# Kernel tuning notes

Measured on AMD Instinct MI355X. Metric: run time of the kernel, lower is better.

The kernel has to match this reference:

```python
import jax, jax.numpy as jnp
import numpy as np

B = 128            # fixed by min(128, len(sample)) loop
NODES_PER_GRAPH = 100
N_NODES = B * NODES_PER_GRAPH
HID = 512          # args.num_hidden
EMB = 1024         # pretrained embedding dim (t_linear in_features)
TWEET_VOCAB = 300000
DESC_VOCAB = 150000
EPS = 1e-5


def setup_inputs() -> dict:
    key = jax.random.key(0)
    ks = jax.random.split(key, 12)
    sample = jnp.stack([
        jax.random.randint(ks[0], (B,), 0, DESC_VOCAB),
        jax.random.randint(ks[1], (B,), 0, TWEET_VOCAB),
        jax.random.randint(ks[2], (B,), 0, DESC_VOCAB),
    ], axis=1)  # [B,3] int
    # sorted node->graph assignment; every graph has >=2 nodes so u_idx+1 is valid
    graph_batch = jnp.repeat(jnp.arange(B), NODES_PER_GRAPH)  # [N_NODES]
    p_feature = jax.random.normal(ks[3], (N_NODES, HID), dtype=jnp.float32)
    tweet_emb = jax.random.normal(ks[4], (TWEET_VOCAB, EMB), dtype=jnp.float32) * 0.02
    desc_emb = jax.random.normal(ks[5], (DESC_VOCAB, EMB), dtype=jnp.float32) * 0.02
    t_w = jax.random.normal(ks[6], (HID, EMB), dtype=jnp.float32) / np.sqrt(EMB)
    t_b = jnp.zeros((HID,), dtype=jnp.float32)
    w1 = jax.random.normal(ks[7], (256, 3 * HID), dtype=jnp.float32) / np.sqrt(3 * HID)
    b1 = jnp.zeros((256,), dtype=jnp.float32)
    gamma = jnp.ones((256,), dtype=jnp.float32)
    beta = jnp.zeros((256,), dtype=jnp.float32)
    w2 = jax.random.normal(ks[8], (1, 256), dtype=jnp.float32) / np.sqrt(256)
    b2 = jnp.zeros((1,), dtype=jnp.float32)
    return {"sample": sample, "graph_batch": graph_batch, "p_feature": p_feature,
            "tweet_emb": tweet_emb, "desc_emb": desc_emb, "t_w": t_w, "t_b": t_b,
            "w1": w1, "b1": b1, "gamma": gamma, "beta": beta, "w2": w2, "b2": b2}


def reference(sample, graph_batch, p_feature, tweet_emb, desc_emb,
              t_w, t_b, w1, b1, gamma, beta, w2, b2):
    # torch.nonzero(batch == i)[0] -> first node index of graph i;
    # graph_batch is sorted, so this is a searchsorted (replaces the 128-iter loop)
    u_idx = jnp.searchsorted(graph_batch, jnp.arange(B))  # [B]
    v_idx = u_idx + 1
    u_feat = p_feature[u_idx]  # [B, HID]
    v_feat = p_feature[v_idx]  # [B, HID]

    t = lambda e: e @ t_w.T + t_b  # Linear(1024 -> HID)
    inp = jnp.concatenate([
        u_feat + t(desc_emb[sample[:, 0]]),
        t(tweet_emb[sample[:, 1]]),
        v_feat + t(desc_emb[sample[:, 2]]),
    ], axis=1)  # [B, 3*HID]

    h = inp @ w1.T + b1  # [B, 256]
    # BatchNorm1d in training mode: biased batch statistics
    mu = jnp.mean(h, axis=0)
    var = jnp.mean((h - mu) ** 2, axis=0)
    h = (h - mu) * jax.lax.rsqrt(var + EPS) * gamma + beta
    # Dropout treated as identity (eval / deterministic reference)
    h = jax.nn.relu(h)
    return jax.nn.sigmoid(h @ w2.T + b2)  # [B, 1]
```

## Files before the change

kernel.cpp:

```cpp
#include <hip/hip_runtime.h>
#include <math.h>

#define BB 128
#define HID 512
#define EMB 1024
#define N1 1536
#define N2 256

typedef __attribute__((ext_vector_type(8))) __bf16 bf16x8;
typedef __attribute__((ext_vector_type(4))) __bf16 bf16x4;
typedef __attribute__((ext_vector_type(4))) float fx4;

#define OFF_ABUF 0
#define OFF_TWB  786432
#define OFF_W1B  1835008
#define OFF_INPB 2621440
#define OFF_P1   3014656
#define OFF_P2   6160384
#define OFF_H    6684672
#define OFF_SC   6815744
#define OFF_SH   6816768
#define OFF_UIDX 6817792

__device__ __forceinline__ fx4 mfma16(bf16x8 a, bf16x8 b, fx4 c) {
    return __builtin_amdgcn_mfma_f32_16x16x32_bf16(a, b, c, 0, 0, 0);
}

__device__ __forceinline__ int lds_idx(int row, int g) {
    return row * 64 + ((g ^ (row & 7)) * 8);
}

__global__ __launch_bounds__(256)
void kA_prep(const int* __restrict__ sample, const int* __restrict__ gb, int n_nodes,
             const float* __restrict__ tweet_emb, const float* __restrict__ desc_emb,
             const float* __restrict__ t_w, const float* __restrict__ w1,
             __bf16* __restrict__ Abuf, __bf16* __restrict__ twb,
             __bf16* __restrict__ w1b, int* __restrict__ uidx)
{
    const int blk = blockIdx.x;
    const int t   = threadIdx.x;

    if (blk < 384) {
        const int s = blk >> 7, b = blk & 127;
        const int id = sample[b * 3 + s];
        const float* src = (s == 1) ? (tweet_emb + (size_t)id * EMB)
                                    : (desc_emb + (size_t)id * EMB);
        float4 v = *(const float4*)(src + t * 4);
        bf16x4 o = {(__bf16)v.x, (__bf16)v.y, (__bf16)v.z, (__bf16)v.w};
        *(bf16x4*)(Abuf + (size_t)blk * EMB + t * 4) = o;
    } else if (blk < 896) {
        const int r = blk - 384;
        float4 v = *(const float4*)(t_w + (size_t)r * EMB + t * 4);
        bf16x4 o = {(__bf16)v.x, (__bf16)v.y, (__bf16)v.z, (__bf16)v.w};
        *(bf16x4*)(twb + (size_t)r * EMB + t * 4) = o;
    } else if (blk < 1152) {
        const int r = blk - 896;
        for (int i = t; i < 384; i += 256) {
            float4 v = *(const float4*)(w1 + (size_t)r * N1 + i * 4);
            bf16x4 o = {(__bf16)v.x, (__bf16)v.y, (__bf16)v.z, (__bf16)v.w};
            *(bf16x4*)(w1b + (size_t)r * N1 + i * 4) = o;
        }
    } else {
        const int n = (blk - 1152) * 256 + t;
        if (n < n_nodes) {
            const int g = gb[n];
            if (n == 0 || gb[n - 1] != g) uidx[g] = n;
        }
    }
}

__global__ __launch_bounds__(256)
void kB_gemm1(const __bf16* __restrict__ Abuf, const __bf16* __restrict__ twb,
              float* __restrict__ part1)
{
    const int n0 = blockIdx.x * 64;
    const int m0 = blockIdx.y * 64;
    const int ks = blockIdx.z;
    const int t  = threadIdx.x;
    const int wid = t >> 6, l = t & 63;
    const int mbase = (wid >> 1) * 32, nbase = (wid & 1) * 32;

    __shared__ __bf16 Alds[64 * 64];
    __shared__ __bf16 Blds[64 * 64];

    const int srow = t >> 2;
    const int g0   = (t & 3) * 2;

    fx4 acc[2][2] = {};

    bf16x8 av0, av1, bv0, bv1;
    {
        const int k0 = ks * 256;
        const __bf16* ap = Abuf + (size_t)(m0 + srow) * EMB + k0 + g0 * 8;
        const __bf16* bp = twb  + (size_t)(n0 + srow) * EMB + k0 + g0 * 8;
        av0 = *(const bf16x8*)ap; av1 = *(const bf16x8*)(ap + 8);
        bv0 = *(const bf16x8*)bp; bv1 = *(const bf16x8*)(bp + 8);
    }

    for (int kt = 0; kt < 4; ++kt) {
        __syncthreads();
        *(bf16x8*)&Alds[lds_idx(srow, g0)]     = av0;
        *(bf16x8*)&Alds[lds_idx(srow, g0 + 1)] = av1;
        *(bf16x8*)&Blds[lds_idx(srow, g0)]     = bv0;
        *(bf16x8*)&Blds[lds_idx(srow, g0 + 1)] = bv1;
        __syncthreads();

        if (kt < 3) {
            const int k0 = ks * 256 + (kt + 1) * 64;
            const __bf16* ap = Abuf + (size_t)(m0 + srow) * EMB + k0 + g0 * 8;
            const __bf16* bp = twb  + (size_t)(n0 + srow) * EMB + k0 + g0 * 8;
            av0 = *(const bf16x8*)ap; av1 = *(const bf16x8*)(ap + 8);
            bv0 = *(const bf16x8*)bp; bv1 = *(const bf16x8*)(bp + 8);
        }

        #pragma unroll
        for (int kq = 0; kq < 2; ++kq) {
            const int g = kq * 4 + (l >> 4);
            bf16x8 a0 = *(const bf16x8*)&Alds[lds_idx(mbase +      (l & 15), g)];
            bf16x8 a1 = *(const bf16x8*)&Alds[lds_idx(mbase + 16 + (l & 15), g)];
            bf16x8 b0 = *(const bf16x8*)&Blds[lds_idx(nbase +      (l & 15), g)];
            bf16x8 b1 = *(const bf16x8*)&Blds[lds_idx(nbase + 16 + (l & 15), g)];
            acc[0][0] = mfma16(a0, b0, acc[0][0]);
            acc[0][1] = mfma16(a0, b1, acc[0][1]);
            acc[1][0] = mfma16(a1, b0, acc[1][0]);
            acc[1][1] = mfma16(a1, b1, acc[1][1]);
        }
    }

    float* dst = part1 + (size_t)ks * (384 * 512);
    #pragma unroll
    for (int mi = 0; mi < 2; ++mi)
        #pragma unroll
        for (int ni = 0; ni < 2; ++ni) {
            const int row = m0 + mbase + mi * 16 + (l >> 4) * 4;
            const int col = n0 + nbase + ni * 16 + (l & 15);
            #pragma unroll
            for (int j = 0; j < 4; ++j)
                dst[(size_t)(row + j) * 512 + col] = acc[mi][ni][j];
        }
}

__global__ __launch_bounds__(256)
void kC_comb1(const float* __restrict__ part1, const float* __restrict__ t_b,
              const float* __restrict__ p_feature, const int* __restrict__ uidx,
              __bf16* __restrict__ inp_bf)
{
    const int t = threadIdx.x;
    const int m = blockIdx.x * 2 + (t >> 7);
    const int j0 = (t & 127) * 4;
    const int s = m >> 7, b = m & 127;

    float4 v = *(const float4*)(part1 + (size_t)m * 512 + j0);
    #pragma unroll
    for (int p = 1; p < 4; ++p) {
        float4 q = *(const float4*)(part1 + (size_t)p * (384 * 512) + (size_t)m * 512 + j0);
        v.x += q.x; v.y += q.y; v.z += q.z; v.w += q.w;
    }
    float4 tb = *(const float4*)(t_b + j0);
    v.x += tb.x; v.y += tb.y; v.z += tb.z; v.w += tb.w;
    if (s != 1) {
        const int node = (s == 0) ? uidx[b] : (uidx[b] + 1);
        float4 pf = *(const float4*)(p_feature + (size_t)node * HID + j0);
        v.x += pf.x; v.y += pf.y; v.z += pf.z; v.w += pf.w;
    }
    bf16x4 o = {(__bf16)v.x, (__bf16)v.y, (__bf16)v.z, (__bf16)v.w};
    *(bf16x4*)(inp_bf + (size_t)m * 512 + j0) = o;
}

__global__ __launch_bounds__(256)
void kD_gemm2(const __bf16* __restrict__ inp_bf, const __bf16* __restrict__ w1b,
              float* __restrict__ part2)
{
    const int n0 = blockIdx.x * 64;
    const int m0 = blockIdx.y * 64;
    const int ks = blockIdx.z;
    const int t  = threadIdx.x;
    const int wid = t >> 6, l = t & 63;
    const int mbase = (wid >> 1) * 32, nbase = (wid & 1) * 32;

    __shared__ __bf16 Alds[64 * 64];
    __shared__ __bf16 Blds[64 * 64];

    const int srow = t >> 2;
    const int g0   = (t & 3) * 2;

    fx4 acc[2][2] = {};

    bf16x8 av0, av1, bv0, bv1;
    {
        const int k0 = ks * 384;
        const __bf16* ap = inp_bf + (size_t)((k0 >> 9) * 128 + m0 + srow) * HID + (k0 & 511) + g0 * 8;
        const __bf16* bp = w1b + (size_t)(n0 + srow) * N1 + k0 + g0 * 8;
        av0 = *(const bf16x8*)ap; av1 = *(const bf16x8*)(ap + 8);
        bv0 = *(const bf16x8*)bp; bv1 = *(const bf16x8*)(bp + 8);
    }

    for (int kt = 0; kt < 6; ++kt) {
        __syncthreads();
        *(bf16x8*)&Alds[lds_idx(srow, g0)]     = av0;
        *(bf16x8*)&Alds[lds_idx(srow, g0 + 1)] = av1;
        *(bf16x8*)&Blds[lds_idx(srow, g0)]     = bv0;
        *(bf16x8*)&Blds[lds_idx(srow, g0 + 1)] = bv1;
        __syncthreads();

        if (kt < 5) {
            const int k0 = ks * 384 + (kt + 1) * 64;
            const __bf16* ap = inp_bf + (size_t)((k0 >> 9) * 128 + m0 + srow) * HID + (k0 & 511) + g0 * 8;
            const __bf16* bp = w1b + (size_t)(n0 + srow) * N1 + k0 + g0 * 8;
            av0 = *(const bf16x8*)ap; av1 = *(const bf16x8*)(ap + 8);
            bv0 = *(const bf16x8*)bp; bv1 = *(const bf16x8*)(bp + 8);
        }

        #pragma unroll
        for (int kq = 0; kq < 2; ++kq) {
            const int g = kq * 4 + (l >> 4);
            bf16x8 a0 = *(const bf16x8*)&Alds[lds_idx(mbase +      (l & 15), g)];
            bf16x8 a1 = *(const bf16x8*)&Alds[lds_idx(mbase + 16 + (l & 15), g)];
            bf16x8 b0 = *(const bf16x8*)&Blds[lds_idx(nbase +      (l & 15), g)];
            bf16x8 b1 = *(const bf16x8*)&Blds[lds_idx(nbase + 16 + (l & 15), g)];
            acc[0][0] = mfma16(a0, b0, acc[0][0]);
            acc[0][1] = mfma16(a0, b1, acc[0][1]);
            acc[1][0] = mfma16(a1, b0, acc[1][0]);
            acc[1][1] = mfma16(a1, b1, acc[1][1]);
        }
    }

    float* dst = part2 + (size_t)ks * (128 * 256);
    #pragma unroll
    for (int mi = 0; mi < 2; ++mi)
        #pragma unroll
        for (int ni = 0; ni < 2; ++ni) {
            const int row = m0 + mbase + mi * 16 + (l >> 4) * 4;
            const int col = n0 + nbase + ni * 16 + (l & 15);
            #pragma unroll
            for (int j = 0; j < 4; ++j)
                dst[(size_t)(row + j) * 256 + col] = acc[mi][ni][j];
        }
}

__global__ __launch_bounds__(256)
void kE_stats(const float* __restrict__ part2, const float* __restrict__ b1,
              const float* __restrict__ gamma, const float* __restrict__ beta,
              float* __restrict__ hbuf, float* __restrict__ scale,
              float* __restrict__ shift)
{
    const int bl = blockIdx.x;
    const int t  = threadIdx.x;
    const int j  = bl * 32 + (t & 31);
    const int q  = t >> 5;

    const float bias = b1[j];
    float sum = 0.f, sq = 0.f;
    for (int i = 0; i < 16; ++i) {
        const int b = q * 16 + i;
        float v = bias;
        #pragma unroll
        for (int p = 0; p < 4; ++p)
            v += part2[(size_t)p * (128 * 256) + b * N2 + j];
        hbuf[b * N2 + j] = v;
        sum += v;
        sq  += v * v;
    }

    __shared__ float s_sum[8][32];
    __shared__ float s_sq[8][32];
    s_sum[q][t & 31] = sum;
    s_sq[q][t & 31]  = sq;
    __syncthreads();

    if (t < 32) {
        float S = 0.f, Q = 0.f;
        #pragma unroll
        for (int q2 = 0; q2 < 8; ++q2) { S += s_sum[q2][t]; Q += s_sq[q2][t]; }
        const float mu  = S * (1.0f / 128.0f);
        const float var = Q * (1.0f / 128.0f) - mu * mu;
        const float rs  = rsqrtf(var + 1e-5f);
        const int jj = bl * 32 + t;
        const float sc = gamma[jj] * rs;
        scale[jj] = sc;
        shift[jj] = beta[jj] - mu * sc;
    }
}

__global__ __launch_bounds__(256)
void kF_out(const float* __restrict__ hbuf, const float* __restrict__ scale,
            const float* __restrict__ shift, const float* __restrict__ w2,
            const float* __restrict__ b2, float* __restrict__ out)
{
    const int t  = threadIdx.x;
    const int wv = t >> 6;
    const int l  = t & 63;
    const int b0 = blockIdx.x * 8 + wv * 2;

    #pragma unroll
    for (int rr = 0; rr < 2; ++rr) {
        const int b = b0 + rr;
        float acc = 0.f;
        #pragma unroll
        for (int i = 0; i < 4; ++i) {
            const int j = l + i * 64;
            float x = hbuf[b * N2 + j] * scale[j] + shift[j];
            x = fmaxf(x, 0.f);
            acc += x * w2[j];
        }
        #pragma unroll
        for (int off = 32; off; off >>= 1) acc += __shfl_xor(acc, off);
        if (l == 0) out[b] = 1.0f / (1.0f + expf(-(acc + b2[0])));
    }
}

extern "C" void kernel_launch(void* const* d_in, const int* in_sizes, int n_in,
                              void* d_out, int out_size, void* d_ws, size_t ws_size,
                              hipStream_t stream) {
    const int*   sample    = (const int*)  d_in[0];
    const int*   gb        = (const int*)  d_in[1];
    const float* p_feature = (const float*)d_in[2];
    const float* tweet_emb = (const float*)d_in[3];
    const float* desc_emb  = (const float*)d_in[4];
    const float* t_w       = (const float*)d_in[5];
    const float* t_b       = (const float*)d_in[6];
    const float* w1        = (const float*)d_in[7];
    const float* b1        = (const float*)d_in[8];
    const float* gamma     = (const float*)d_in[9];
    const float* beta      = (const float*)d_in[10];
    const float* w2        = (const float*)d_in[11];
    const float* b2        = (const float*)d_in[12];
    float* out = (float*)d_out;

    char* ws = (char*)d_ws;
    __bf16* Abuf   = (__bf16*)(ws + OFF_ABUF);
    __bf16* twb    = (__bf16*)(ws + OFF_TWB);
    __bf16* w1b    = (__bf16*)(ws + OFF_W1B);
    __bf16* inp_bf = (__bf16*)(ws + OFF_INPB);
    float*  part1  = (float*)(ws + OFF_P1);
    float*  part2  = (float*)(ws + OFF_P2);
    float*  hbuf   = (float*)(ws + OFF_H);
    float*  scale  = (float*)(ws + OFF_SC);
    float*  shift  = (float*)(ws + OFF_SH);
    int*    uidx   = (int*)  (ws + OFF_UIDX);

    const int n_nodes = in_sizes[1];
    const int scatter_blocks = (n_nodes + 255) / 256;

    kA_prep<<<1152 + scatter_blocks, 256, 0, stream>>>(sample, gb, n_nodes,
        tweet_emb, desc_emb, t_w, w1, Abuf, twb, w1b, uidx);
    kB_gemm1<<<dim3(8, 6, 4), 256, 0, stream>>>(Abuf, twb, part1);
    kC_comb1<<<192, 256, 0, stream>>>(part1, t_b, p_feature, uidx, inp_bf);
    kD_gemm2<<<dim3(4, 2, 4), 256, 0, stream>>>(inp_bf, w1b, part2);
    kE_stats<<<8, 256, 0, stream>>>(part2, b1, gamma, beta, hbuf, scale, shift);
    kF_out<<<16, 256, 0, stream>>>(hbuf, scale, shift, w2, b2, out);
}
```

Measured before the change: 27.79 us.

## Fuse bf16 conversion, gather and bias epilogue into GEMM kernels

Measured after the change: 43.60 us. 56.9% more time.

```diff
diff --git a/kernel.cpp b/kernel.cpp
--- a/kernel.cpp
+++ b/kernel.cpp
@@ -1,26 +1,18 @@
 #include <hip/hip_runtime.h>
 #include <math.h>
 
-#define BB 128
 #define HID 512
 #define EMB 1024
 #define N1 1536
 #define N2 256
 
 typedef __attribute__((ext_vector_type(8))) __bf16 bf16x8;
-typedef __attribute__((ext_vector_type(4))) __bf16 bf16x4;
 typedef __attribute__((ext_vector_type(4))) float fx4;
 
-#define OFF_ABUF 0
-#define OFF_TWB  786432
-#define OFF_W1B  1835008
-#define OFF_INPB 2621440
-#define OFF_P1   3014656
-#define OFF_P2   6160384
-#define OFF_H    6684672
-#define OFF_SC   6815744
-#define OFF_SH   6816768
-#define OFF_UIDX 6817792
+#define OFF_INPB 0
+#define OFF_P2   393216
+#define OFF_SC   917504
+#define OFF_SH   918528
 
 __device__ __forceinline__ fx4 mfma16(bf16x8 a, bf16x8 b, fx4 c) {
     return __builtin_amdgcn_mfma_f32_16x16x32_bf16(a, b, c, 0, 0, 0);
@@ -30,74 +22,66 @@
     return row * 64 + ((g ^ (row & 7)) * 8);
 }
 
+__device__ __forceinline__ bf16x8 cvt8(float4 a, float4 b) {
+    bf16x8 r;
+    r[0] = (__bf16)a.x; r[1] = (__bf16)a.y; r[2] = (__bf16)a.z; r[3] = (__bf16)a.w;
+    r[4] = (__bf16)b.x; r[5] = (__bf16)b.y; r[6] = (__bf16)b.z; r[7] = (__bf16)b.w;
+    return r;
+}
+
 __global__ __launch_bounds__(256)
-void kA_prep(const int* __restrict__ sample, const int* __restrict__ gb, int n_nodes,
-             const float* __restrict__ tweet_emb, const float* __restrict__ desc_emb,
-             const float* __restrict__ t_w, const float* __restrict__ w1,
-             __bf16* __restrict__ Abuf, __bf16* __restrict__ twb,
-             __bf16* __restrict__ w1b, int* __restrict__ uidx)
-{
-    const int blk = blockIdx.x;
-    const int t   = threadIdx.x;
-
-    if (blk < 384) {
-        const int s = blk >> 7, b = blk & 127;
-        const int id = sample[b * 3 + s];
-        const float* src = (s == 1) ? (tweet_emb + (size_t)id * EMB)
-                                    : (desc_emb + (size_t)id * EMB);
-        float4 v = *(const float4*)(src + t * 4);
-        bf16x4 o = {(__bf16)v.x, (__bf16)v.y, (__bf16)v.z, (__bf16)v.w};
-        *(bf16x4*)(Abuf + (size_t)blk * EMB + t * 4) = o;
-    } else if (blk < 896) {
-        const int r = blk - 384;
-        float4 v = *(const float4*)(t_w + (size_t)r * EMB + t * 4);
-        bf16x4 o = {(__bf16)v.x, (__bf16)v.y, (__bf16)v.z, (__bf16)v.w};
-        *(bf16x4*)(twb + (size_t)r * EMB + t * 4) = o;
-    } else if (blk < 1152) {
-        const int r = blk - 896;
-        for (int i = t; i < 384; i += 256) {
-            float4 v = *(const float4*)(w1 + (size_t)r * N1 + i * 4);
-            bf16x4 o = {(__bf16)v.x, (__bf16)v.y, (__bf16)v.z, (__bf16)v.w};
-            *(bf16x4*)(w1b + (size_t)r * N1 + i * 4) = o;
-        }
-    } else {
-        const int n = (blk - 1152) * 256 + t;
-        if (n < n_nodes) {
-            const int g = gb[n];
-            if (n == 0 || gb[n - 1] != g) uidx[g] = n;
-        }
-    }
-}
-
-__global__ __launch_bounds__(256)
-void kB_gemm1(const __bf16* __restrict__ Abuf, const __bf16* __restrict__ twb,
-              float* __restrict__ part1)
+void kG1(const int* __restrict__ sample, const int* __restrict__ gb, int n_nodes,
+         const float* __restrict__ p_feature,
+         const float* __restrict__ tweet_emb, const float* __restrict__ desc_emb,
+         const float* __restrict__ t_w, const float* __restrict__ t_b,
+         __bf16* __restrict__ inp_bf)
 {
     const int n0 = blockIdx.x * 64;
     const int m0 = blockIdx.y * 64;
-    const int ks = blockIdx.z;
+    const int s  = m0 >> 7;
+    const int b0 = m0 & 127;
     const int t  = threadIdx.x;
     const int wid = t >> 6, l = t & 63;
     const int mbase = (wid >> 1) * 32, nbase = (wid & 1) * 32;
 
     __shared__ __bf16 Alds[64 * 64];
     __shared__ __bf16 Blds[64 * 64];
+    __shared__ int node_lds[64];
+
+    if (s != 1) {
+        for (int n = t; n < n_nodes; n += 256) {
+            const int g = gb[n];
+            const int rel = g - b0;
+            if (rel >= 0 && rel < 64) {
+                if (n == 0 || gb[n - 1] != g) node_lds[rel] = n;
+            }
+        }
+    }
 
     const int srow = t >> 2;
+    const int c0   = (t & 3) * 16;
     const int g0   = (t & 3) * 2;
 
+    const int bb  = b0 + srow;
+    const int sid = sample[bb * 3 + s];
+    const float* erow = ((s == 1) ? tweet_emb : desc_emb) + (size_t)sid * EMB;
+    const float* wrow = t_w + (size_t)(n0 + srow) * EMB;
+
     fx4 acc[2][2] = {};
 
-    bf16x8 av0, av1, bv0, bv1;
+    float4 pa0, pa1, pa2, pa3, pb0, pb1, pb2, pb3;
     {
-        const int k0 = ks * 256;
-        const __bf16* ap = Abuf + (size_t)(m0 + srow) * EMB + k0 + g0 * 8;
-        const __bf16* bp = twb  + (size_t)(n0 + srow) * EMB + k0 + g0 * 8;
-        av0 = *(const bf16x8*)ap; av1 = *(const bf16x8*)(ap + 8);
-        bv0 = *(const bf16x8*)bp; bv1 = *(const bf16x8*)(bp + 8);
-    }
-
-    for (int kt = 0; kt < 4; ++kt) {
+        const float* a = erow + c0;
+        const float* b = wrow + c0;
+        pa0 = *(const float4*)(a);      pa1 = *(const float4*)(a + 4);
+        pa2 = *(const float4*)(a + 8);  pa3 = *(const float4*)(a + 12);
+        pb0 = *(const float4*)(b);      pb1 = *(const float4*)(b + 4);
+        pb2 = *(const float4*)(b + 8);  pb3 = *(const float4*)(b + 12);
+    }
+
+    for (int kt = 0; kt < 16; ++kt) {
+        bf16x8 av0 = cvt8(pa0, pa1), av1 = cvt8(pa2, pa3);
+        bf16x8 bv0 = cvt8(pb0, pb1), bv1 = cvt8(pb2, pb3);
         __syncthreads();
         *(bf16x8*)&Alds[lds_idx(srow, g0)]     = av0;
         *(bf16x8*)&Alds[lds_idx(srow, g0 + 1)] = av1;
@@ -105,12 +89,13 @@
         *(bf16x8*)&Blds[lds_idx(srow, g0 + 1)] = bv1;
         __syncthreads();
 
-        if (kt < 3) {
-            const int k0 = ks * 256 + (kt + 1) * 64;
-            const __bf16* ap = Abuf + (size_t)(m0 + srow) * EMB + k0 + g0 * 8;
-            const __bf16* bp = twb  + (size_t)(n0 + srow) * EMB + k0 + g0 * 8;
-            av0 = *(const bf16x8*)ap; av1 = *(const bf16x8*)(ap + 8);
-            bv0 = *(const bf16x8*)bp; bv1 = *(const bf16x8*)(bp + 8);
+        if (kt < 15) {
+            const float* a = erow + (kt + 1) * 64 + c0;
+            const float* b = wrow + (kt + 1) * 64 + c0;
+            pa0 = *(const float4*)(a);      pa1 = *(const float4*)(a + 4);
+            pa2 = *(const float4*)(a + 8);  pa3 = *(const float4*)(a + 12);
+            pb0 = *(const float4*)(b);      pb1 = *(const float4*)(b + 4);
+            pb2 = *(const float4*)(b + 8);  pb3 = *(const float4*)(b + 12);
         }
 
         #pragma unroll
@@ -127,49 +112,30 @@
         }
     }
 
-    float* dst = part1 + (size_t)ks * (384 * 512);
+    const int addv = (s == 2) ? 1 : 0;
     #pragma unroll
     for (int mi = 0; mi < 2; ++mi)
         #pragma unroll
         for (int ni = 0; ni < 2; ++ni) {
             const int row = m0 + mbase + mi * 16 + (l >> 4) * 4;
             const int col = n0 + nbase + ni * 16 + (l & 15);
+            const float tb = t_b[col];
             #pragma unroll
-            for (int j = 0; j < 4; ++j)
-                dst[(size_t)(row + j) * 512 + col] = acc[mi][ni][j];
+            for (int j = 0; j < 4; ++j) {
+                const int r = row + j;
+                float v = acc[mi][ni][j] + tb;
+                if (s != 1) {
+                    const int node = node_lds[r - m0] + addv;
+                    v += p_feature[(size_t)node * HID + col];
+                }
+                inp_bf[(size_t)r * HID + col] = (__bf16)v;
+            }
         }
 }
 
 __global__ __launch_bounds__(256)
-void kC_comb1(const float* __restrict__ part1, const float* __restrict__ t_b,
-              const float* __restrict__ p_feature, const int* __restrict__ uidx,
-              __bf16* __restrict__ inp_bf)
-{
-    const int t = threadIdx.x;
-    const int m = blockIdx.x * 2 + (t >> 7);
-    const int j0 = (t & 127) * 4;
-    const int s = m >> 7, b = m & 127;
-
-    float4 v = *(const float4*)(part1 + (size_t)m * 512 + j0);
-    #pragma unroll
-    for (int p = 1; p < 4; ++p) {
-        float4 q = *(const float4*)(part1 + (size_t)p * (384 * 512) + (size_t)m * 512 + j0);
-        v.x += q.x; v.y += q.y; v.z += q.z; v.w += q.w;
-    }
-    float4 tb = *(const float4*)(t_b + j0);
-    v.x += tb.x; v.y += tb.y; v.z += tb.z; v.w += tb.w;
-    if (s != 1) {
-        const int node = (s == 0) ? uidx[b] : (uidx[b] + 1);
-        float4 pf = *(const float4*)(p_feature + (size_t)node * HID + j0);
-        v.x += pf.x; v.y += pf.y; v.z += pf.z; v.w += pf.w;
-    }
-    bf16x4 o = {(__bf16)v.x, (__bf16)v.y, (__bf16)v.z, (__bf16)v.w};
-    *(bf16x4*)(inp_bf + (size_t)m * 512 + j0) = o;
-}
-
-__global__ __launch_bounds__(256)
-void kD_gemm2(const __bf16* __restrict__ inp_bf, const __bf16* __restrict__ w1b,
-              float* __restrict__ part2)
+void kG2(const __bf16* __restrict__ inp_bf, const float* __restrict__ w1,
+         float* __restrict__ part2)
 {
     const int n0 = blockIdx.x * 64;
     const int m0 = blockIdx.y * 64;
@@ -182,20 +148,26 @@
     __shared__ __bf16 Blds[64 * 64];
 
     const int srow = t >> 2;
+    const int c0   = (t & 3) * 16;
     const int g0   = (t & 3) * 2;
 
+    const float* wrow = w1 + (size_t)(n0 + srow) * N1;
+
     fx4 acc[2][2] = {};
 
-    bf16x8 av0, av1, bv0, bv1;
+    bf16x8 av0, av1;
+    float4 pb0, pb1, pb2, pb3;
     {
         const int k0 = ks * 384;
-        const __bf16* ap = inp_bf + (size_t)((k0 >> 9) * 128 + m0 + srow) * HID + (k0 & 511) + g0 * 8;
-        const __bf16* bp = w1b + (size_t)(n0 + srow) * N1 + k0 + g0 * 8;
+        const __bf16* ap = inp_bf + (size_t)(((k0 >> 9) * 128) + m0 + srow) * HID + (k0 & 511) + c0;
         av0 = *(const bf16x8*)ap; av1 = *(const bf16x8*)(ap + 8);
-        bv0 = *(const bf16x8*)bp; bv1 = *(const bf16x8*)(bp + 8);
+        const float* b = wrow + k0 + c0;
+        pb0 = *(const float4*)(b);      pb1 = *(const float4*)(b + 4);
+        pb2 = *(const float4*)(b + 8);  pb3 = *(const float4*)(b + 12);
     }
 
     for (int kt = 0; kt < 6; ++kt) {
+        bf16x8 bv0 = cvt8(pb0, pb1), bv1 = cvt8(pb2, pb3);
         __syncthreads();
         *(bf16x8*)&Alds[lds_idx(srow, g0)]     = av0;
         *(bf16x8*)&Alds[lds_idx(srow, g0 + 1)] = av1;
@@ -205,10 +177,11 @@
 
         if (kt < 5) {
             const int k0 = ks * 384 + (kt + 1) * 64;
-            const __bf16* ap = inp_bf + (size_t)((k0 >> 9) * 128 + m0 + srow) * HID + (k0 & 511) + g0 * 8;
-            const __bf16* bp = w1b + (size_t)(n0 + srow) * N1 + k0 + g0 * 8;
+            const __bf16* ap = inp_bf + (size_t)(((k0 >> 9) * 128) + m0 + srow) * HID + (k0 & 511) + c0;
             av0 = *(const bf16x8*)ap; av1 = *(const bf16x8*)(ap + 8);
-            bv0 = *(const bf16x8*)bp; bv1 = *(const bf16x8*)(bp + 8);
+            const float* b = wrow + k0 + c0;
+            pb0 = *(const float4*)(b);      pb1 = *(const float4*)(b + 4);
+            pb2 = *(const float4*)(b + 8);  pb3 = *(const float4*)(b + 12);
         }
 
         #pragma unroll
@@ -234,15 +207,14 @@
             const int col = n0 + nbase + ni * 16 + (l & 15);
             #pragma unroll
             for (int j = 0; j < 4; ++j)
-                dst[(size_t)(row + j) * 256 + col] = acc[mi][ni][j];
+                dst[(size_t)(row + j) * N2 + col] = acc[mi][ni][j];
         }
 }
 
 __global__ __launch_bounds__(256)
-void kE_stats(const float* __restrict__ part2, const float* __restrict__ b1,
-              const float* __restrict__ gamma, const float* __restrict__ beta,
-              float* __restrict__ hbuf, float* __restrict__ scale,
-              float* __restrict__ shift)
+void kS(const float* __restrict__ part2, const float* __restrict__ b1,
+        const float* __restrict__ gamma, const float* __restrict__ beta,
+        float* __restrict__ scale, float* __restrict__ shift)
 {
     const int bl = blockIdx.x;
     const int t  = threadIdx.x;
@@ -257,7 +229,6 @@
         #pragma unroll
         for (int p = 0; p < 4; ++p)
             v += part2[(size_t)p * (128 * 256) + b * N2 + j];
-        hbuf[b * N2 + j] = v;
         sum += v;
         sq  += v * v;
     }
@@ -283,9 +254,10 @@
 }
 
 __global__ __launch_bounds__(256)
-void kF_out(const float* __restrict__ hbuf, const float* __restrict__ scale,
-            const float* __restrict__ shift, const float* __restrict__ w2,
-            const float* __restrict__ b2, float* __restrict__ out)
+void kO(const float* __restrict__ part2, const float* __restrict__ b1,
+        const float* __restrict__ scale, const float* __restrict__ shift,
+        const float* __restrict__ w2, const float* __restrict__ b2,
+        float* __restrict__ out)
 {
     const int t  = threadIdx.x;
     const int wv = t >> 6;
@@ -299,7 +271,11 @@
         #pragma unroll
         for (int i = 0; i < 4; ++i) {
             const int j = l + i * 64;
-            float x = hbuf[b * N2 + j] * scale[j] + shift[j];
+            float v = b1[j];
+            #pragma unroll
+            for (int p = 0; p < 4; ++p)
+                v += part2[(size_t)p * (128 * 256) + b * N2 + j];
+            float x = v * scale[j] + shift[j];
             x = fmaxf(x, 0.f);
             acc += x * w2[j];
         }
@@ -328,25 +304,15 @@
     float* out = (float*)d_out;
 
     char* ws = (char*)d_ws;
-    __bf16* Abuf   = (__bf16*)(ws + OFF_ABUF);
-    __bf16* twb    = (__bf16*)(ws + OFF_TWB);
-    __bf16* w1b    = (__bf16*)(ws + OFF_W1B);
     __bf16* inp_bf = (__bf16*)(ws + OFF_INPB);
-    float*  part1  = (float*)(ws + OFF_P1);
     float*  part2  = (float*)(ws + OFF_P2);
-    float*  hbuf   = (float*)(ws + OFF_H);
     float*  scale  = (float*)(ws + OFF_SC);
     float*  shift  = (float*)(ws + OFF_SH);
-    int*    uidx   = (int*)  (ws + OFF_UIDX);
-
     const int n_nodes = in_sizes[1];
-    const int scatter_blocks = (n_nodes + 255) / 256;
-
-    kA_prep<<<1152 + scatter_blocks, 256, 0, stream>>>(sample, gb, n_nodes,
-        tweet_emb, desc_emb, t_w, w1, Abuf, twb, w1b, uidx);
-    kB_gemm1<<<dim3(8, 6, 4), 256, 0, stream>>>(Abuf, twb, part1);
-    kC_comb1<<<192, 256, 0, stream>>>(part1, t_b, p_feature, uidx, inp_bf);
-    kD_gemm2<<<dim3(4, 2, 4), 256, 0, stream>>>(inp_bf, w1b, part2);
-    kE_stats<<<8, 256, 0, stream>>>(part2, b1, gamma, beta, hbuf, scale, shift);
-    kF_out<<<16, 256, 0, stream>>>(hbuf, scale, shift, w2, b2, out);
-}
+
+    kG1<<<dim3(8, 6), 256, 0, stream>>>(sample, gb, n_nodes, p_feature,
+                                        tweet_emb, desc_emb, t_w, t_b, inp_bf);
+    kG2<<<dim3(4, 2, 4), 256, 0, stream>>>(inp_bf, w1, part2);
+    kS<<<8, 256, 0, stream>>>(part2, b1, gamma, beta, scale, shift);
+    kO<<<16, 256, 0, stream>>>(part2, b1, scale, shift, w2, b2, out);
+}
```

## Fuse GEMM and epilogue kernels using atomic-counter grid barriers

Applied to the files above, without the earlier changes.

After: 62.83 us. 126% more time.

```diff
diff --git a/kernel.cpp b/kernel.cpp
--- a/kernel.cpp
+++ b/kernel.cpp
@@ -1,7 +1,6 @@
 #include <hip/hip_runtime.h>
 #include <math.h>
 
-#define BB 128
 #define HID 512
 #define EMB 1024
 #define N1 1536
@@ -17,10 +16,10 @@
 #define OFF_INPB 2621440
 #define OFF_P1   3014656
 #define OFF_P2   6160384
-#define OFF_H    6684672
-#define OFF_SC   6815744
-#define OFF_SH   6816768
-#define OFF_UIDX 6817792
+#define OFF_SC   6684672
+#define OFF_SH   6685696
+#define OFF_UIDX 6686720
+#define OFF_CTR  6687232
 
 __device__ __forceinline__ fx4 mfma16(bf16x8 a, bf16x8 b, fx4 c) {
     return __builtin_amdgcn_mfma_f32_16x16x32_bf16(a, b, c, 0, 0, 0);
@@ -30,15 +29,28 @@
     return row * 64 + ((g ^ (row & 7)) * 8);
 }
 
+__device__ __forceinline__ void gsync(int* ctr, int target) {
+    __threadfence();
+    __syncthreads();
+    if (threadIdx.x == 0) {
+        atomicAdd(ctr, 1);
+        while (atomicAdd(ctr, 0) < target) __builtin_amdgcn_s_sleep(2);
+        __threadfence();
+    }
+    __syncthreads();
+}
+
 __global__ __launch_bounds__(256)
-void kA_prep(const int* __restrict__ sample, const int* __restrict__ gb, int n_nodes,
-             const float* __restrict__ tweet_emb, const float* __restrict__ desc_emb,
-             const float* __restrict__ t_w, const float* __restrict__ w1,
-             __bf16* __restrict__ Abuf, __bf16* __restrict__ twb,
-             __bf16* __restrict__ w1b, int* __restrict__ uidx)
+void kPrep(const int* __restrict__ sample, const int* __restrict__ gb, int n_nodes,
+           const float* __restrict__ tweet_emb, const float* __restrict__ desc_emb,
+           const float* __restrict__ t_w, const float* __restrict__ w1,
+           __bf16* __restrict__ Abuf, __bf16* __restrict__ twb,
+           __bf16* __restrict__ w1b, int* __restrict__ uidx, int* __restrict__ ctr)
 {
     const int blk = blockIdx.x;
     const int t   = threadIdx.x;
+
+    if (blk == 0 && t < 3) ctr[t] = 0;
 
     if (blk < 384) {
         const int s = blk >> 7, b = blk & 127;
@@ -70,8 +82,10 @@
 }
 
 __global__ __launch_bounds__(256)
-void kB_gemm1(const __bf16* __restrict__ Abuf, const __bf16* __restrict__ twb,
-              float* __restrict__ part1)
+void kFused1(const __bf16* __restrict__ Abuf, const __bf16* __restrict__ twb,
+             const float* __restrict__ t_b, const float* __restrict__ p_feature,
+             const int* __restrict__ uidx, float* __restrict__ part1,
+             __bf16* __restrict__ inp_bf, int* __restrict__ ctr)
 {
     const int n0 = blockIdx.x * 64;
     const int m0 = blockIdx.y * 64;
@@ -127,179 +141,170 @@
         }
     }
 
-    float* dst = part1 + (size_t)ks * (384 * 512);
-    #pragma unroll
-    for (int mi = 0; mi < 2; ++mi)
-        #pragma unroll
-        for (int ni = 0; ni < 2; ++ni) {
-            const int row = m0 + mbase + mi * 16 + (l >> 4) * 4;
-            const int col = n0 + nbase + ni * 16 + (l & 15);
-            #pragma unroll
-            for (int j = 0; j < 4; ++j)
-                dst[(size_t)(row + j) * 512 + col] = acc[mi][ni][j];
-        }
+    {
+        float* dst = part1 + (size_t)ks * (384 * 512);
+        #pragma unroll
+        for (int mi = 0; mi < 2; ++mi)
+            #pragma unroll
+            for (int ni = 0; ni < 2; ++ni) {
+                const int row = m0 + mbase + mi * 16 + (l >> 4) * 4;
+                const int col = n0 + nbase + ni * 16 + (l & 15);
+                #pragma unroll
+                for (int j = 0; j < 4; ++j)
+                    dst[(size_t)(row + j) * 512 + col] = acc[mi][ni][j];
+            }
+    }
+
+    gsync(ctr, 192);
+
+    {
+        const int lid = blockIdx.x + 8 * blockIdx.y + 48 * blockIdx.z;
+        const int m = lid * 2 + (t >> 7);
+        const int j0 = (t & 127) * 4;
+        const int s = m >> 7, b = m & 127;
+
+        float4 v = *(const float4*)(part1 + (size_t)m * 512 + j0);
+        #pragma unroll
+        for (int p = 1; p < 4; ++p) {
+            float4 q = *(const float4*)(part1 + (size_t)p * (384 * 512) + (size_t)m * 512 + j0);
+            v.x += q.x; v.y += q.y; v.z += q.z; v.w += q.w;
+        }
+        float4 tb = *(const float4*)(t_b + j0);
+        v.x += tb.x; v.y += tb.y; v.z += tb.z; v.w += tb.w;
+        if (s != 1) {
+            const int node = (s == 0) ? uidx[b] : (uidx[b] + 1);
+            float4 pf = *(const float4*)(p_feature + (size_t)node * HID + j0);
+            v.x += pf.x; v.y += pf.y; v.z += pf.z; v.w += pf.w;
+        }
+        bf16x4 o = {(__bf16)v.x, (__bf16)v.y, (__bf16)v.z, (__bf16)v.w};
+        *(bf16x4*)(inp_bf + (size_t)m * 512 + j0) = o;
+    }
 }
 
 __global__ __launch_bounds__(256)
-void kC_comb1(const float* __restrict__ part1, const float* __restrict__ t_b,
-              const float* __restrict__ p_feature, const int* __restrict__ uidx,
-              __bf16* __restrict__ inp_bf)
+void kFused2(const __bf16* __restrict__ inp_bf, const __bf16* __restrict__ w1b,
+             const float* __restrict__ b1, const float* __restrict__ gamma,
+             const float* __restrict__ beta, const float* __restrict__ w2,
+             const float* __restrict__ b2, float* __restrict__ part2,
+             float* __restrict__ scale, float* __restrict__ shift,
+             float* __restrict__ out, int* __restrict__ ctr2, int* __restrict__ ctr3)
 {
-    const int t = threadIdx.x;
-    const int m = blockIdx.x * 2 + (t >> 7);
-    const int j0 = (t & 127) * 4;
-    const int s = m >> 7, b = m & 127;
-
-    float4 v = *(const float4*)(part1 + (size_t)m * 512 + j0);
-    #pragma unroll
-    for (int p = 1; p < 4; ++p) {
-        float4 q = *(const float4*)(part1 + (size_t)p * (384 * 512) + (size_t)m * 512 + j0);
-        v.x += q.x; v.y += q.y; v.z += q.z; v.w += q.w;
-    }
-    float4 tb = *(const float4*)(t_b + j0);
-    v.x += tb.x; v.y += tb.y; v.z += tb.z; v.w += tb.w;
-    if (s != 1) {
-        const int node = (s == 0) ? uidx[b] : (uidx[b] + 1);
-        float4 pf = *(const float4*)(p_feature + (size_t)node * HID + j0);
-        v.x += pf.x; v.y += pf.y; v.z += pf.z; v.w += pf.w;
-    }
-    bf16x4 o = {(__bf16)v.x, (__bf16)v.y, (__bf16)v.z, (__bf16)v.w};
-    *(bf16x4*)(inp_bf + (size_t)m * 512 + j0) = o;
-}
-
-__global__ __launch_bounds__(256)
-void kD_gemm2(const __bf16* __restrict__ inp_bf, const __bf16* __restrict__ w1b,
-              float* __restrict__ part2)
-{
-    const int n0 = blockIdx.x * 64;
-    const int m0 = blockIdx.y * 64;
-    const int ks = blockIdx.z;
-    const int t  = threadIdx.x;
-    const int wid = t >> 6, l = t & 63;
-    const int mbase = (wid >> 1) * 32, nbase = (wid & 1) * 32;
-
-    __shared__ __bf16 Alds[64 * 64];
-    __shared__ __bf16 Blds[64 * 64];
-
-    const int srow = t >> 2;
-    const int g0   = (t & 3) * 2;
-
-    fx4 acc[2][2] = {};
-
-    bf16x8 av0, av1, bv0, bv1;
-    {
-        const int k0 = ks * 384;
-        const __bf16* ap = inp_bf + (size_t)((k0 >> 9) * 128 + m0 + srow) * HID + (k0 & 511) + g0 * 8;
-        const __bf16* bp = w1b + (size_t)(n0 + srow) * N1 + k0 + g0 * 8;
-        av0 = *(const bf16x8*)ap; av1 = *(const bf16x8*)(ap + 8);
-        bv0 = *(const bf16x8*)bp; bv1 = *(const bf16x8*)(bp + 8);
-    }
-
-    for (int kt = 0; kt < 6; ++kt) {
-        __syncthreads();
-        *(bf16x8*)&Alds[lds_idx(srow, g0)]     = av0;
-        *(bf16x8*)&Alds[lds_idx(srow, g0 + 1)] = av1;
-        *(bf16x8*)&Blds[lds_idx(srow, g0)]     = bv0;
-        *(bf16x8*)&Blds[lds_idx(srow, g0 + 1)] = bv1;
-        __syncthreads();
-
-        if (kt < 5) {
-            const int k0 = ks * 384 + (kt + 1) * 64;
-            const __bf16* ap = inp_bf + (size_t)((k0 >> 9) * 128 + m0 + srow) * HID + (k0 & 511) + g0 * 8;
+    const int blk = blockIdx.x;
+    const int t   = threadIdx.x;
+
+    {
+        const int n0 = (blk & 3) * 64;
+        const int m0 = ((blk >> 2) & 1) * 64;
+        const int ks = blk >> 3;
+        const int wid = t >> 6, l = t & 63;
+        const int mbase = (wid >> 1) * 32, nbase = (wid & 1) * 32;
+
+        __shared__ __bf16 Alds[64 * 64];
+        __shared__ __bf16 Blds[64 * 64];
+
+        const int srow = t >> 2;
+        const int g0   = (t & 3) * 2;
+
+        fx4 acc[2][2] = {};
+
+        bf16x8 av0, av1, bv0, bv1;
+        {
+            const int k0 = ks * 384;
+            const __bf16* ap = inp_bf + (size_t)(((k0 >> 9) * 128) + m0 + srow) * HID + (k0 & 511) + g0 * 8;
             const __bf16* bp = w1b + (size_t)(n0 + srow) * N1 + k0 + g0 * 8;
             av0 = *(const bf16x8*)ap; av1 = *(const bf16x8*)(ap + 8);
             bv0 = *(const bf16x8*)bp; bv1 = *(const bf16x8*)(bp + 8);
         }
 
-        #pragma unroll
-        for (int kq = 0; kq < 2; ++kq) {
-            const int g = kq * 4 + (l >> 4);
-            bf16x8 a0 = *(const bf16x8*)&Alds[lds_idx(mbase +      (l & 15), g)];
-            bf16x8 a1 = *(const bf16x8*)&Alds[lds_idx(mbase + 16 + (l & 15), g)];
-            bf16x8 b0 = *(const bf16x8*)&Blds[lds_idx(nbase +      (l & 15), g)];
-            bf16x8 b1 = *(const bf16x8*)&Blds[lds_idx(nbase + 16 + (l & 15), g)];
-            acc[0][0] = mfma16(a0, b0, acc[0][0]);
-            acc[0][1] = mfma16(a0, b1, acc[0][1]);
-            acc[1][0] = mfma16(a1, b0, acc[1][0]);
-            acc[1][1] = mfma16(a1, b1, acc[1][1]);
-        }
-    }
-
-    float* dst = part2 + (size_t)ks * (128 * 256);
-    #pragma unroll
-    for (int mi = 0; mi < 2; ++mi)
-        #pragma unroll
-        for (int ni = 0; ni < 2; ++ni) {
-            const int row = m0 + mbase + mi * 16 + (l >> 4) * 4;
-            const int col = n0 + nbase + ni * 16 + (l & 15);
-            #pragma unroll
-            for (int j = 0; j < 4; ++j)
-                dst[(size_t)(row + j) * 256 + col] = acc[mi][ni][j];
-        }
-}
-
-__global__ __launch_bounds__(256)
-void kE_stats(const float* __restrict__ part2, const float* __restrict__ b1,
-              const float* __restrict__ gamma, const float* __restrict__ beta,
-              float* __restrict__ hbuf, float* __restrict__ scale,
-              float* __restrict__ shift)
-{
-    const int bl = blockIdx.x;
-    const int t  = threadIdx.x;
-    const int j  = bl * 32 + (t & 31);
-    const int q  = t >> 5;
-
-    const float bias = b1[j];
-    float sum = 0.f, sq = 0.f;
-    for (int i = 0; i < 16; ++i) {
-        const int b = q * 16 + i;
-        float v = bias;
-        #pragma unroll
-        for (int p = 0; p < 4; ++p)
-            v += part2[(size_t)p * (128 * 256) + b * N2 + j];
-        hbuf[b * N2 + j] = v;
-        sum += v;
-        sq  += v * v;
-    }
-
-    __shared__ float s_sum[8][32];
-    __shared__ float s_sq[8][32];
-    s_sum[q][t & 31] = sum;
-    s_sq[q][t & 31]  = sq;
-    __syncthreads();
-
-    if (t < 32) {
-        float S = 0.f, Q = 0.f;
-        #pragma unroll
-        for (int q2 = 0; q2 < 8; ++q2) { S += s_sum[q2][t]; Q += s_sq[q2][t]; }
-        const float mu  = S * (1.0f / 128.0f);
-        const float var = Q * (1.0f / 128.0f) - mu * mu;
-        const float rs  = rsqrtf(var + 1e-5f);
-        const int jj = bl * 32 + t;
-        const float sc = gamma[jj] * rs;
-        scale[jj] = sc;
-        shift[jj] = beta[jj] - mu * sc;
-    }
-}
-
-__global__ __launch_bounds__(256)
-void kF_out(const float* __restrict__ hbuf, const float* __restrict__ scale,
-            const float* __restrict__ shift, const float* __restrict__ w2,
-            const float* __restrict__ b2, float* __restrict__ out)
-{
-    const int t  = threadIdx.x;
-    const int wv = t >> 6;
-    const int l  = t & 63;
-    const int b0 = blockIdx.x * 8 + wv * 2;
-
-    #pragma unroll
-    for (int rr = 0; rr < 2; ++rr) {
-        const int b = b0 + rr;
+        for (int kt = 0; kt < 6; ++kt) {
+            __syncthreads();
+            *(bf16x8*)&Alds[lds_idx(srow, g0)]     = av0;
+            *(bf16x8*)&Alds[lds_idx(srow, g0 + 1)] = av1;
+            *(bf16x8*)&Blds[lds_idx(srow, g0)]     = bv0;
+            *(bf16x8*)&Blds[lds_idx(srow, g0 + 1)] = bv1;
+            __syncthreads();
+
+            if (kt < 5) {
+                const int k0 = ks * 384 + (kt + 1) * 64;
+                const __bf16* ap = inp_bf + (size_t)(((k0 >> 9) * 128) + m0 + srow) * HID + (k0 & 511) + g0 * 8;
+                const __bf16* bp = w1b + (size_t)(n0 + srow) * N1 + k0 + g0 * 8;
+                av0 = *(const bf16x8*)ap; av1 = *(const bf16x8*)(ap + 8);
+                bv0 = *(const bf16x8*)bp; bv1 = *(const bf16x8*)(bp + 8);
+            }
+
+            #pragma unroll
+            for (int kq = 0; kq < 2; ++kq) {
+                const int g = kq * 4 + (l >> 4);
+                bf16x8 a0 = *(const bf16x8*)&Alds[lds_idx(mbase +      (l & 15), g)];
+                bf16x8 a1 = *(const bf16x8*)&Alds[lds_idx(mbase + 16 + (l & 15), g)];
+                bf16x8 b0 = *(const bf16x8*)&Blds[lds_idx(nbase +      (l & 15), g)];
+                bf16x8 b1 = *(const bf16x8*)&Blds[lds_idx(nbase + 16 + (l & 15), g)];
+                acc[0][0] = mfma16(a0, b0, acc[0][0]);
+                acc[0][1] = mfma16(a0, b1, acc[0][1]);
+                acc[1][0] = mfma16(a1, b0, acc[1][0]);
+                acc[1][1] = mfma16(a1, b1, acc[1][1]);
+            }
+        }
+
+        float* dst = part2 + (size_t)ks * (128 * 256);
+        #pragma unroll
+        for (int mi = 0; mi < 2; ++mi)
+            #pragma unroll
+            for (int ni = 0; ni < 2; ++ni) {
+                const int row = m0 + mbase + mi * 16 + (l >> 4) * 4;
+                const int col = n0 + nbase + ni * 16 + (l & 15);
+                #pragma unroll
+                for (int j = 0; j < 4; ++j)
+                    dst[(size_t)(row + j) * N2 + col] = acc[mi][ni][j];
+            }
+    }
+
+    gsync(ctr2, 32);
+
+    {
+        const int j = blk * 8 + (t >> 5);
+        const int r = t & 31;
+        const float bias = b1[j];
+        float sum = 0.f, sq = 0.f;
+        #pragma unroll
+        for (int i = 0; i < 4; ++i) {
+            const int row = r + i * 32;
+            float v = bias;
+            #pragma unroll
+            for (int p = 0; p < 4; ++p)
+                v += part2[(size_t)p * (128 * 256) + row * N2 + j];
+            sum += v;
+            sq  += v * v;
+        }
+        #pragma unroll
+        for (int off = 16; off; off >>= 1) {
+            sum += __shfl_xor(sum, off);
+            sq  += __shfl_xor(sq, off);
+        }
+        if (r == 0) {
+            const float mu  = sum * (1.0f / 128.0f);
+            const float var = sq * (1.0f / 128.0f) - mu * mu;
+            const float rs  = rsqrtf(var + 1e-5f);
+            const float sc  = gamma[j] * rs;
+            scale[j] = sc;
+            shift[j] = beta[j] - mu * sc;
+        }
+    }
+
+    gsync(ctr3, 32);
+
+    {
+        const int b = blk * 4 + (t >> 6);
+        const int l = t & 63;
         float acc = 0.f;
         #pragma unroll
         for (int i = 0; i < 4; ++i) {
             const int j = l + i * 64;
-            float x = hbuf[b * N2 + j] * scale[j] + shift[j];
+            float v = b1[j];
+            #pragma unroll
+            for (int p = 0; p < 4; ++p)
+                v += part2[(size_t)p * (128 * 256) + b * N2 + j];
+            float x = v * scale[j] + shift[j];
             x = fmaxf(x, 0.f);
             acc += x * w2[j];
         }
@@ -334,19 +339,18 @@
     __bf16* inp_bf = (__bf16*)(ws + OFF_INPB);
     float*  part1  = (float*)(ws + OFF_P1);
     float*  part2  = (float*)(ws + OFF_P2);
-    float*  hbuf   = (float*)(ws + OFF_H);
     float*  scale  = (float*)(ws + OFF_SC);
     float*  shift  = (float*)(ws + OFF_SH);
     int*    uidx   = (int*)  (ws + OFF_UIDX);
+    int*    ctr    = (int*)  (ws + OFF_CTR);
 
     const int n_nodes = in_sizes[1];
     const int scatter_blocks = (n_nodes + 255) / 256;
 
-    kA_prep<<<1152 + scatter_blocks, 256, 0, stream>>>(sample, gb, n_nodes,
-        tweet_emb, desc_emb, t_w, w1, Abuf, twb, w1b, uidx);
-    kB_gemm1<<<dim3(8, 6, 4), 256, 0, stream>>>(Abuf, twb, part1);
-    kC_comb1<<<192, 256, 0, stream>>>(part1, t_b, p_feature, uidx, inp_bf);
-    kD_gemm2<<<dim3(4, 2, 4), 256, 0, stream>>>(inp_bf, w1b, part2);
-    kE_stats<<<8, 256, 0, stream>>>(part2, b1, gamma, beta, hbuf, scale, shift);
-    kF_out<<<16, 256, 0, stream>>>(hbuf, scale, shift, w2, b2, out);
-}
+    kPrep<<<1152 + scatter_blocks, 256, 0, stream>>>(sample, gb, n_nodes,
+        tweet_emb, desc_emb, t_w, w1, Abuf, twb, w1b, uidx, ctr);
+    kFused1<<<dim3(8, 6, 4), 256, 0, stream>>>(Abuf, twb, t_b, p_feature, uidx,
+                                               part1, inp_bf, ctr + 0);
+    kFused2<<<32, 256, 0, stream>>>(inp_bf, w1b, b1, gamma, beta, w2, b2,
+                                    part2, scale, shift, out, ctr + 1, ctr + 2);
+}
```
